# Kernel tuning notes

Hardware: AMD Instinct MI355X
Metric: run time of the kernel (lower is better)

## Reference

```python
import jax, jax.numpy as jnp
import numpy as np

K_SPARSE = 64  # number of units kept active per row

def setup_inputs() -> dict:
    key = jax.random.key(0)
    x = jax.random.normal(key, (16384, 4096), dtype=jnp.float32)
    return {"x": x}

def reference(x) -> jnp.ndarray:
    # Training-phase path of KSparse.call -> k_sparsify:
    # kth_smallest = sort(x)[..., n-1-k]  (the (k+1)-th largest value per row)
    # out = x * (x > kth_smallest)
    n = x.shape[-1]
    sorted_x = jnp.sort(x, axis=-1)              # ascending, [B, D]
    kth = sorted_x[:, n - 1 - K_SPARSE]          # [B]
    mask = (x > kth[:, None]).astype(x.dtype)    # strictly greater, as in source
    return x * mask
```

## Files before the change

### kernel.cpp

```cpp
#include <hip/hip_runtime.h>

#define K_SPARSE 64
#define COLS     4096
#define NTHREADS 128
#define EPT      (COLS / NTHREADS)
#define VPT      (EPT / 4)
#define FAST_CAP 1024
#define LIST_CAP (FAST_CAP + 8)

typedef float    nfloat4 __attribute__((ext_vector_type(4)));
typedef unsigned nuint4  __attribute__((ext_vector_type(4)));

__device__ __forceinline__ unsigned mapf(unsigned b) {
    return (b & 0x80000000u) ? ~b : (b | 0x80000000u);
}
__device__ __forceinline__ float unmapf(unsigned u) {
    unsigned b = (u & 0x80000000u) ? (u ^ 0x80000000u) : ~u;
    return __uint_as_float(b);
}

__global__ __launch_bounds__(NTHREADS, 8)
void ksparse_select(const float* __restrict__ x, float* __restrict__ out, int rows)
{
    const int row = blockIdx.x;
    if (row >= rows) return;
    const int t    = threadIdx.x;
    const int lane = t & 63;
    const int w    = t >> 6;

    __shared__ __align__(16) unsigned list[LIST_CAP];
    __shared__ unsigned wtot[2];
    __shared__ unsigned s_kth;

    const float4* __restrict__ xrow =
        reinterpret_cast<const float4*>(x) + (size_t)row * (COLS / 4);
    nfloat4* __restrict__ orow =
        reinterpret_cast<nfloat4*>(out) + (size_t)row * (COLS / 4);

    unsigned u[EPT];
#pragma unroll
    for (int i = 0; i < VPT; ++i) {
        float4 v = xrow[t + i * NTHREADS];
        u[i * 4 + 0] = mapf(__float_as_uint(v.x));
        u[i * 4 + 1] = mapf(__float_as_uint(v.y));
        u[i * 4 + 2] = mapf(__float_as_uint(v.z));
        u[i * 4 + 3] = mapf(__float_as_uint(v.w));
    }

    unsigned uT = 0, cnt = 0, base = 0, c = 0;
    for (int r = 0; r < 4; ++r) {
        uT = (r == 0) ? 0xBFF33333u
           : (r == 1) ? 0xBF666666u
           : (r == 2) ? 0x00800000u : 0u;
        cnt = 0;
#pragma unroll
        for (int i = 0; i < EPT; ++i) cnt += (u[i] > uT) ? 1u : 0u;

        unsigned s = cnt;
#pragma unroll
        for (int off = 1; off < 64; off <<= 1) {
            unsigned v = __shfl_up(s, off, 64);
            if (lane >= off) s += v;
        }
        if (lane == 63) wtot[w] = s;
        __syncthreads();
        const unsigned c0 = wtot[0], c1 = wtot[1];
        c = c0 + c1;
        if (c >= K_SPARSE + 1 || r == 3) {
            base = (w > 0 ? c0 : 0u) + s - cnt;
            break;
        }
        __syncthreads();
    }

    unsigned ukth;
    if (c >= K_SPARSE + 1 && c <= FAST_CAP) {
        unsigned pos = base;
#pragma unroll
        for (int i = 0; i < EPT; ++i) {
            if (u[i] > uT) list[pos++] = u[i];
        }
        if (t < 8) list[c + t] = 0u;
        __syncthreads();

        const int nq = (int)((c + 3) >> 2);
        const nuint4* listv = reinterpret_cast<const nuint4*>(list);
        for (int j = t; j < (int)c; j += NTHREADS) {
            const unsigned vj = list[j];
            unsigned g = 0, e = 0;
            for (int q = 0; q < nq; ++q) {
                const nuint4 ql = listv[q];
                g += (ql.x > vj) + (ql.y > vj) + (ql.z > vj) + (ql.w > vj);
                e += (ql.x == vj) + (ql.y == vj) + (ql.z == vj) + (ql.w == vj);
            }
            if (g <= (unsigned)K_SPARSE && (unsigned)K_SPARSE < g + e)
                s_kth = vj;
        }
        __syncthreads();
        ukth = s_kth;
    } else {
        unsigned prefix = 0u;
        for (int b = 31; b >= 0; --b) {
            const unsigned trial = prefix | (1u << b);
            unsigned c2 = 0;
#pragma unroll
            for (int i = 0; i < EPT; ++i) c2 += (u[i] >= trial) ? 1u : 0u;
#pragma unroll
            for (int off = 32; off >= 1; off >>= 1)
                c2 += __shfl_xor(c2, off, 64);
            if (lane == 0) wtot[w] = c2;
            __syncthreads();
            const unsigned tot = wtot[0] + wtot[1];
            if (tot >= K_SPARSE + 1) prefix = trial;
            __syncthreads();
        }
        ukth = prefix;
    }

#pragma unroll
    for (int i = 0; i < VPT; ++i) {
        nfloat4 o;
        o.x = (u[i * 4 + 0] > ukth) ? unmapf(u[i * 4 + 0]) : 0.0f;
        o.y = (u[i * 4 + 1] > ukth) ? unmapf(u[i * 4 + 1]) : 0.0f;
        o.z = (u[i * 4 + 2] > ukth) ? unmapf(u[i * 4 + 2]) : 0.0f;
        o.w = (u[i * 4 + 3] > ukth) ? unmapf(u[i * 4 + 3]) : 0.0f;
        __builtin_nontemporal_store(o, &orow[t + i * NTHREADS]);
    }
}

extern "C" void kernel_launch(void* const* d_in, const int* in_sizes, int n_in,
                              void* d_out, int out_size, void* d_ws, size_t ws_size,
                              hipStream_t stream) {
    const float* x = (const float*)d_in[0];
    float* out = (float*)d_out;
    const int rows = in_sizes[0] / COLS;
    ksparse_select<<<rows, NTHREADS, 0, stream>>>(x, out, rows);
}
```

Measured before the change: 79.41 us.

## Process one row per wavefront to replace block barriers with wave intrinsics

Each 64-lane wavefront now handles a whole row, with four rows per 256-thread block. Shared-memory counters and __syncthreads are replaced by shuffles and a ballot to pick the k-th value. Each thread holds 64 elements in registers instead of 32, which raises register pressure and may lower occupancy. The pre-threshold rounds drop from four to two and the fast-path list capacity shrinks, so rare rows fall back to the bitwise radix search.

```diff
diff --git a/kernel.cpp b/kernel.cpp
--- a/kernel.cpp
+++ b/kernel.cpp
@@ -2,11 +2,12 @@
 
 #define K_SPARSE 64
 #define COLS     4096
-#define NTHREADS 128
-#define EPT      (COLS / NTHREADS)
+#define NTHREADS 256
+#define WAVES    4
+#define EPT      64
 #define VPT      (EPT / 4)
-#define FAST_CAP 1024
-#define LIST_CAP (FAST_CAP + 8)
+#define FAST_CAP 512
+#define LPAD     (FAST_CAP + 8)
 
 typedef float    nfloat4 __attribute__((ext_vector_type(4)));
 typedef unsigned nuint4  __attribute__((ext_vector_type(4)));
@@ -19,18 +20,17 @@
     return __uint_as_float(b);
 }
 
-__global__ __launch_bounds__(NTHREADS, 8)
-void ksparse_select(const float* __restrict__ x, float* __restrict__ out, int rows)
+__global__ __launch_bounds__(NTHREADS)
+void ksparse_wave(const float* __restrict__ x, float* __restrict__ out, int rows)
 {
-    const int row = blockIdx.x;
-    if (row >= rows) return;
     const int t    = threadIdx.x;
     const int lane = t & 63;
     const int w    = t >> 6;
+    const int row  = blockIdx.x * WAVES + w;
+    if (row >= rows) return;
 
-    __shared__ __align__(16) unsigned list[LIST_CAP];
-    __shared__ unsigned wtot[2];
-    __shared__ unsigned s_kth;
+    __shared__ __align__(16) unsigned list[WAVES][LPAD];
+    unsigned* const lw = list[w];
 
     const float4* __restrict__ xrow =
         reinterpret_cast<const float4*>(x) + (size_t)row * (COLS / 4);
@@ -40,7 +40,7 @@
     unsigned u[EPT];
 #pragma unroll
     for (int i = 0; i < VPT; ++i) {
-        float4 v = xrow[t + i * NTHREADS];
+        float4 v = xrow[lane + i * 64];
         u[i * 4 + 0] = mapf(__float_as_uint(v.x));
         u[i * 4 + 1] = mapf(__float_as_uint(v.y));
         u[i * 4 + 2] = mapf(__float_as_uint(v.z));
@@ -48,10 +48,9 @@
     }
 
     unsigned uT = 0, cnt = 0, base = 0, c = 0;
-    for (int r = 0; r < 4; ++r) {
-        uT = (r == 0) ? 0xBFF33333u
-           : (r == 1) ? 0xBF666666u
-           : (r == 2) ? 0x00800000u : 0u;
+#pragma unroll
+    for (int r = 0; r < 2; ++r) {
+        uT = (r == 0) ? 0xBFF33333u : 0xBFC00000u;
         cnt = 0;
 #pragma unroll
         for (int i = 0; i < EPT; ++i) cnt += (u[i] > uT) ? 1u : 0u;
@@ -62,15 +61,9 @@
             unsigned v = __shfl_up(s, off, 64);
             if (lane >= off) s += v;
         }
-        if (lane == 63) wtot[w] = s;
-        __syncthreads();
-        const unsigned c0 = wtot[0], c1 = wtot[1];
-        c = c0 + c1;
-        if (c >= K_SPARSE + 1 || r == 3) {
-            base = (w > 0 ? c0 : 0u) + s - cnt;
-            break;
-        }
-        __syncthreads();
+        c    = __shfl(s, 63, 64);
+        base = s - cnt;
+        if (c >= K_SPARSE + 1) break;
     }
 
     unsigned ukth;
@@ -78,26 +71,29 @@
         unsigned pos = base;
 #pragma unroll
         for (int i = 0; i < EPT; ++i) {
-            if (u[i] > uT) list[pos++] = u[i];
+            if (u[i] > uT) lw[pos++] = u[i];
         }
-        if (t < 8) list[c + t] = 0u;
-        __syncthreads();
+        if (lane < 8) lw[c + lane] = 0u;
 
         const int nq = (int)((c + 3) >> 2);
-        const nuint4* listv = reinterpret_cast<const nuint4*>(list);
-        for (int j = t; j < (int)c; j += NTHREADS) {
-            const unsigned vj = list[j];
+        const nuint4* lv = reinterpret_cast<const nuint4*>(lw);
+        bool found = false;
+        unsigned vmatch = 0u;
+        for (int j = lane; j < (int)c; j += 64) {
+            const unsigned vj = lw[j];
             unsigned g = 0, e = 0;
             for (int q = 0; q < nq; ++q) {
-                const nuint4 ql = listv[q];
+                const nuint4 ql = lv[q];
                 g += (ql.x > vj) + (ql.y > vj) + (ql.z > vj) + (ql.w > vj);
                 e += (ql.x == vj) + (ql.y == vj) + (ql.z == vj) + (ql.w == vj);
             }
-            if (g <= (unsigned)K_SPARSE && (unsigned)K_SPARSE < g + e)
-                s_kth = vj;
+            if (g <= (unsigned)K_SPARSE && (unsigned)K_SPARSE < g + e) {
+                found = true; vmatch = vj;
+            }
         }
-        __syncthreads();
-        ukth = s_kth;
+        const unsigned long long m = __ballot(found);
+        const int src = __ffsll(m) - 1;
+        ukth = __shfl(vmatch, src, 64);
     } else {
         unsigned prefix = 0u;
         for (int b = 31; b >= 0; --b) {
@@ -108,11 +104,7 @@
 #pragma unroll
             for (int off = 32; off >= 1; off >>= 1)
                 c2 += __shfl_xor(c2, off, 64);
-            if (lane == 0) wtot[w] = c2;
-            __syncthreads();
-            const unsigned tot = wtot[0] + wtot[1];
-            if (tot >= K_SPARSE + 1) prefix = trial;
-            __syncthreads();
+            if (c2 >= K_SPARSE + 1) prefix = trial;
         }
         ukth = prefix;
     }
@@ -124,7 +116,7 @@
         o.y = (u[i * 4 + 1] > ukth) ? unmapf(u[i * 4 + 1]) : 0.0f;
         o.z = (u[i * 4 + 2] > ukth) ? unmapf(u[i * 4 + 2]) : 0.0f;
         o.w = (u[i * 4 + 3] > ukth) ? unmapf(u[i * 4 + 3]) : 0.0f;
-        __builtin_nontemporal_store(o, &orow[t + i * NTHREADS]);
+        __builtin_nontemporal_store(o, &orow[lane + i * 64]);
     }
 }
 
@@ -134,5 +126,6 @@
     const float* x = (const float*)d_in[0];
     float* out = (float*)d_out;
     const int rows = in_sizes[0] / COLS;
-    ksparse_select<<<rows, NTHREADS, 0, stream>>>(x, out, rows);
+    const int blocks = (rows + WAVES - 1) / WAVES;
+    ksparse_wave<<<blocks, NTHREADS, 0, stream>>>(x, out, rows);
 }
```

Result: slower. 81.23 us (+2.3%).
